# Kernel optimization log

Measured on AMD Instinct MI355X. Metric: run time of the kernel, lower is better.

The kernel has to match this reference:

```python
import jax, jax.numpy as jnp
import numpy as np

N_NODES = 100000


def gcn_conv(x, W, b, src, dst, n_nodes):
    # PyG GCNConv: x' = D^{-1/2} (A + I) D^{-1/2} (x W) + b, deg counts self-loops
    h = x @ W  # [N, out]
    deg = jax.ops.segment_sum(jnp.ones_like(dst, dtype=h.dtype), dst, num_segments=n_nodes) + 1.0
    dinv = jax.lax.rsqrt(deg)  # [N]
    norm = dinv[src] * dinv[dst]  # per-edge norm [E]
    msg = h[src] * norm[:, None]  # gather + scale, [E, out]
    agg = jax.ops.segment_sum(msg, dst, num_segments=n_nodes)
    agg = agg + h * (dinv * dinv)[:, None]  # self-loop contribution
    return agg + b


def setup_inputs() -> dict:
    key = jax.random.key(0)
    ks = jax.random.split(key, 9)
    N, E, D = N_NODES, 3200000, 165
    x = jax.random.normal(ks[0], (N, D), dtype=jnp.float32)
    edge_index = jax.random.randint(ks[1], (2, E), 0, N, dtype=jnp.int64)
    def glorot(k, fan_in, fan_out):
        lim = np.sqrt(6.0 / (fan_in + fan_out))
        return jax.random.uniform(k, (fan_in, fan_out), jnp.float32, -lim, lim)
    return {
        "x": x,
        "edge_index": edge_index,
        "W1": glorot(ks[2], D, 32), "b1": jnp.zeros((32,), jnp.float32),
        "W2": glorot(ks[3], 32, 16), "b2": jnp.zeros((16,), jnp.float32),
        "W3": glorot(ks[4], 16, 2),  "b3": jnp.zeros((2,), jnp.float32),
    }


def reference(x, edge_index, W1, b1, W2, b2, W3, b3):
    src, dst = edge_index[0], edge_index[1]
    n = x.shape[0]
    h = jax.nn.relu(gcn_conv(x, W1, b1, src, dst, n))
    # dropout p=0.3 is a no-op in eval mode (training=False)
    h = jax.nn.relu(gcn_conv(h, W2, b2, src, dst, n))
    h = gcn_conv(h, W3, b3, src, dst, n)
    return jax.nn.log_softmax(h, axis=1)
```

## Files before the change

### kernel.cpp

```cpp
#include <hip/hip_runtime.h>
#include <math.h>


constexpr int NT = 256;
constexpr int NPB = 256;
constexpr int LOG_NPB = 8;
constexpr int MAXBUK = 512;
constexpr int BSTRIDE = 10240;
constexpr int NREP = 8;
constexpr int SUB = BSTRIDE / NREP;
constexpr int EPB_B = 4096;
constexpr int R = 8;
constexpr int RSH = 14;

typedef __attribute__((ext_vector_type(8))) short bf16x8;
typedef __attribute__((ext_vector_type(4))) float f32x4;

__device__ inline unsigned short f2bf(float f) {
    unsigned u = *(unsigned*)&f;
    u += 0x7fffu + ((u >> 16) & 1u);
    return (unsigned short)(u >> 16);
}
__device__ inline unsigned packbf(float a, float b) {
    return (unsigned)f2bf(a) | ((unsigned)f2bf(b) << 16);
}
__device__ inline void acc8(float* a, uint4 v) {
    const unsigned* u = (const unsigned*)&v;
#pragma unroll
    for (int w = 0; w < 4; w++) {
        unsigned lo = u[w] << 16, hi = u[w] & 0xffff0000u;
        a[2 * w]     += *(float*)&lo;
        a[2 * w + 1] += *(float*)&hi;
    }
}

__global__ __launch_bounds__(NT) void place_kernel(const int* __restrict__ src,
                                                   const int* __restrict__ dst,
                                                   int* __restrict__ cursor8,
                                                   unsigned* __restrict__ ebuf,
                                                   int E, int nbuk) {
    __shared__ int lh[MAXBUK];
    __shared__ int lbase[MAXBUK];
    for (int i = threadIdx.x; i < nbuk; i += NT) lh[i] = 0;
    __syncthreads();
    constexpr int EPT = EPB_B / NT;
    unsigned pk[EPT];
    unsigned bl[EPT];
    int base = blockIdx.x * EPB_B;
    int rep = blockIdx.x & (NREP - 1);
#pragma unroll
    for (int i = 0; i < EPT; i++) {
        int e = base + i * NT + threadIdx.x;
        if (e < E) {
            int s = src[e], d = dst[e];
            int b = d >> LOG_NPB;
            int lp = atomicAdd(&lh[b], 1);
            pk[i] = ((unsigned)(d & (NPB - 1)) << 24) | (unsigned)s;
            bl[i] = ((unsigned)b << 16) | (unsigned)lp;
        } else {
            bl[i] = 0xFFFFFFFFu;
        }
    }
    __syncthreads();
    for (int i = threadIdx.x; i < nbuk; i += NT) {
        int v = lh[i];
        if (v) lbase[i] = atomicAdd(&cursor8[rep * MAXBUK + i], v);
    }
    __syncthreads();
#pragma unroll
    for (int i = 0; i < EPT; i++) {
        if (bl[i] != 0xFFFFFFFFu) {
            int b = (int)(bl[i] >> 16);
            int pos = lbase[b] + (int)(bl[i] & 0xFFFFu);
            if (pos < SUB)
                ebuf[(size_t)b * BSTRIDE + rep * SUB + pos] = pk[i];
        }
    }
}

__global__ __launch_bounds__(NT) void sort_kernel(
    const unsigned* __restrict__ ebuf, const int* __restrict__ cursor8,
    int* __restrict__ esrc, int* __restrict__ rowptr, int* __restrict__ rowcnt,
    float* __restrict__ dinv, int N) {
    __shared__ unsigned se[BSTRIDE];
    __shared__ int cnt[NPB * R];
    __shared__ int cur[NPB * R];
    __shared__ int psum[NT];
    int tid = threadIdx.x;
    int b = blockIdx.x;
    for (int i = tid; i < NPB * R; i += NT) cnt[i] = 0;
    __syncthreads();
    int scnt[NREP], sofs[NREP];
    int total = 0;
#pragma unroll
    for (int r = 0; r < NREP; r++) {
        int v = min(cursor8[r * MAXBUK + b], SUB);
        scnt[r] = v; sofs[r] = total; total += v;
    }
#pragma unroll
    for (int r = 0; r < NREP; r++) {
        int e0 = b * BSTRIDE + r * SUB;
        for (int i = tid; i < scnt[r]; i += NT) {
            unsigned p = ebuf[e0 + i];
            se[sofs[r] + i] = p;
            atomicAdd(&cnt[(p >> 24) * R + ((p & 0xFFFFFFu) >> RSH)], 1);
        }
    }
    __syncthreads();
    int loc[R];
    int s = 0;
#pragma unroll
    for (int i = 0; i < R; i++) { loc[i] = s; s += cnt[tid * R + i]; }
    psum[tid] = s;
    __syncthreads();
    for (int off = 1; off < NPB; off <<= 1) {
        int a = (tid >= off) ? psum[tid - off] : 0;
        __syncthreads();
        psum[tid] += a;
        __syncthreads();
    }
    int excl = psum[tid] - s;
#pragma unroll
    for (int i = 0; i < R; i++) cur[tid * R + i] = excl + loc[i];
    {
        int n = b * NPB + tid;
        if (n < N) {
            rowptr[n] = b * BSTRIDE + excl;
            rowcnt[n] = s;
            dinv[n] = rsqrtf((float)s + 1.0f);
        }
    }
    __syncthreads();
    for (int i = tid; i < total; i += NT) {
        unsigned p = se[i];
        unsigned sidx = p & 0xFFFFFFu;
        int bin = (int)(p >> 24) * R + (int)(sidx >> RSH);
        int pos = atomicAdd(&cur[bin], 1);
        esrc[b * BSTRIDE + pos] = (int)sidx;
    }
}

__global__ __launch_bounds__(NT) void gemm1_mfma(
    const float* __restrict__ in, const float* __restrict__ W,
    const float* __restrict__ dinv, uint4* __restrict__ hs, int Ntot) {
    constexpr int DIN = 165;
    constexpr int RP = 200;
    __shared__ unsigned short xs[64 * RP];
    __shared__ unsigned short ws[32 * RP];
    __shared__ float tile[4][16][36];
    int ntiles = (Ntot + 15) >> 4;
    int slab0 = (blockIdx.x * 4) << 4;
    int rows = min(64, Ntot - slab0);
    for (int i = threadIdx.x; i < (64 + 32) * (RP - DIN); i += NT) {
        int r = i / (RP - DIN);
        int k = DIN + (i - r * (RP - DIN));
        if (r < 64) xs[r * RP + k] = 0;
        else        ws[(r - 64) * RP + k] = 0;
    }
    {
        const float* xbase = in + (size_t)slab0 * DIN;
        int tot = rows * DIN;
        for (int i = threadIdx.x; i < tot; i += NT) {
            int r = i / DIN;
            xs[i + r * (RP - DIN)] = f2bf(xbase[i]);
        }
    }
    for (int i = threadIdx.x; i < DIN * 32; i += NT) {
        int k = i >> 5;
        int col = i & 31;
        ws[col * RP + k] = f2bf(W[i]);
    }
    __syncthreads();
    int lane = threadIdx.x & 63;
    int wv = threadIdx.x >> 6;
    int t = blockIdx.x * 4 + wv;
    if (t >= ntiles) return;
    int n0 = t << 4;
    int mrow = lane & 15;
    int quad = lane >> 4;
    int arow = n0 + mrow;
    if (arow >= Ntot) arow = Ntot - 1;
    int lrow = arow - slab0;
    f32x4 acc0 = {0.f, 0.f, 0.f, 0.f};
    f32x4 acc1 = {0.f, 0.f, 0.f, 0.f};
#pragma unroll
    for (int c = 0; c < 6; c++) {
        int kb = c * 32 + quad * 8;
        union { bf16x8 v; unsigned short u[8]; } A, B0, B1;
        __builtin_memcpy(&A.v,  &xs[lrow * RP + kb], 16);
        __builtin_memcpy(&B0.v, &ws[mrow * RP + kb], 16);
        __builtin_memcpy(&B1.v, &ws[(16 + mrow) * RP + kb], 16);
        acc0 = __builtin_amdgcn_mfma_f32_16x16x32_bf16(A.v, B0.v, acc0, 0, 0, 0);
        acc1 = __builtin_amdgcn_mfma_f32_16x16x32_bf16(A.v, B1.v, acc1, 0, 0, 0);
    }
#pragma unroll
    for (int r = 0; r < 4; r++) {
        tile[wv][quad * 4 + r][mrow] = acc0[r];
        tile[wv][quad * 4 + r][16 + mrow] = acc1[r];
    }
    int node = lane >> 2;
    int part = lane & 3;
    int n = n0 + node;
    if (n >= Ntot) return;
    float dv = dinv[n];
    float f[8];
#pragma unroll
    for (int i = 0; i < 8; i++) f[i] = tile[wv][node][part * 8 + i];
    unsigned u0 = packbf(dv * f[0], dv * f[1]);
    unsigned u1 = packbf(dv * f[2], dv * f[3]);
    unsigned u2 = packbf(dv * f[4], dv * f[5]);
    unsigned u3 = packbf(dv * f[6], dv * f[7]);
    hs[(size_t)n * 4 + part] = make_uint4(u0, u1, u2, u3);
}

__global__ __launch_bounds__(NT) void g1g2_kernel(
    const uint4* __restrict__ hsb, const int* __restrict__ esrc,
    const int* __restrict__ rowptr, const int* __restrict__ rowcnt,
    const float* __restrict__ dinv, const float* __restrict__ b1,
    const float* __restrict__ W2 , uint4* __restrict__ hs2b,
    int N) {
    __shared__ float sW[32 * 16];
    __shared__ float sb[32];
    for (int i = threadIdx.x; i < 32 * 16; i += NT) sW[i] = W2[i];
    if (threadIdx.x < 32) sb[threadIdx.x] = b1[threadIdx.x];
    __syncthreads();
    int gid = blockIdx.x * NT + threadIdx.x;
    int n = gid >> 2;
    int q = gid & 3;
    int c = q & 1;
    int h = q >> 1;
    if (n >= N) return;
    int start = rowptr[n];
    int cnt = rowcnt[n];
    int half0 = (cnt + 1) >> 1;
    int j    = start + (h ? half0 : 0);
    int jend = start + (h ? cnt : half0);
    float a[16];
    if (h == 0) {
        const uint4* hp = hsb + (size_t)n * 4 + c * 2;
        uint4 v0 = hp[0], v1 = hp[1];
        const unsigned* u0 = (const unsigned*)&v0;
        const unsigned* u1 = (const unsigned*)&v1;
#pragma unroll
        for (int w = 0; w < 4; w++) {
            unsigned lo = u0[w] << 16, hi = u0[w] & 0xffff0000u;
            a[2 * w] = *(float*)&lo; a[2 * w + 1] = *(float*)&hi;
            unsigned lo1 = u1[w] << 16, hi1 = u1[w] & 0xffff0000u;
            a[8 + 2 * w] = *(float*)&lo1; a[8 + 2 * w + 1] = *(float*)&hi1;
        }
    } else {
#pragma unroll
        for (int k = 0; k < 16; k++) a[k] = 0.f;
    }
    for (; j + 3 < jend; j += 4) {
        int s0 = esrc[j], s1 = esrc[j + 1], s2 = esrc[j + 2], s3 = esrc[j + 3];
        uint4 v00 = hsb[(size_t)s0 * 4 + c * 2], v01 = hsb[(size_t)s0 * 4 + c * 2 + 1];
        uint4 v10 = hsb[(size_t)s1 * 4 + c * 2], v11 = hsb[(size_t)s1 * 4 + c * 2 + 1];
        uint4 v20 = hsb[(size_t)s2 * 4 + c * 2], v21 = hsb[(size_t)s2 * 4 + c * 2 + 1];
        uint4 v30 = hsb[(size_t)s3 * 4 + c * 2], v31 = hsb[(size_t)s3 * 4 + c * 2 + 1];
        acc8(a, v00); acc8(a + 8, v01);
        acc8(a, v10); acc8(a + 8, v11);
        acc8(a, v20); acc8(a + 8, v21);
        acc8(a, v30); acc8(a + 8, v31);
    }
    for (; j < jend; j++) {
        int s = esrc[j];
        acc8(a, hsb[(size_t)s * 4 + c * 2]);
        acc8(a + 8, hsb[(size_t)s * 4 + c * 2 + 1]);
    }
#pragma unroll
    for (int k = 0; k < 16; k++) a[k] += __shfl_xor(a[k], 2);
    float dv = dinv[n];
    float z[16];
#pragma unroll
    for (int d = 0; d < 16; d++) z[d] = 0.f;
#pragma unroll
    for (int k = 0; k < 16; k++) {
        float f = fmaxf(fmaf(dv, a[k], sb[c * 16 + k]), 0.f);
#pragma unroll
        for (int d = 0; d < 16; d++)
            z[d] = fmaf(f, sW[(c * 16 + k) * 16 + d], z[d]);
    }
#pragma unroll
    for (int d = 0; d < 16; d++) z[d] += __shfl_xor(z[d], 1);
    if (h == 0) {
        unsigned u0 = packbf(dv * z[c * 8 + 0], dv * z[c * 8 + 1]);
        unsigned u1 = packbf(dv * z[c * 8 + 2], dv * z[c * 8 + 3]);
        unsigned u2 = packbf(dv * z[c * 8 + 4], dv * z[c * 8 + 5]);
        unsigned u3 = packbf(dv * z[c * 8 + 6], dv * z[c * 8 + 7]);
        hs2b[(size_t)n * 2 + c] = make_uint4(u0, u1, u2, u3);
    }
}

__global__ __launch_bounds__(NT) void g2g3_kernel(
    const uint4* __restrict__ hs2b, const int* __restrict__ esrc,
    const int* __restrict__ rowptr, const int* __restrict__ rowcnt,
    const float* __restrict__ dinv, const float* __restrict__ b2,
    const float* __restrict__ W3 , float* __restrict__ hs3,
    int N) {
    __shared__ float sW[32];
    __shared__ float sb[16];
    if (threadIdx.x < 32) sW[threadIdx.x] = W3[threadIdx.x];
    if (threadIdx.x < 16) sb[threadIdx.x] = b2[threadIdx.x];
    __syncthreads();
    int gid = blockIdx.x * NT + threadIdx.x;
    int n = gid >> 2;
    int q = gid & 3;
    int c = q & 1;
    int h = q >> 1;
    if (n >= N) return;
    int start = rowptr[n];
    int cnt = rowcnt[n];
    int half0 = (cnt + 1) >> 1;
    int j    = start + (h ? half0 : 0);
    int jend = start + (h ? cnt : half0);
    float a[8];
    if (h == 0) {
        uint4 v = hs2b[(size_t)n * 2 + c];
        const unsigned* u = (const unsigned*)&v;
#pragma unroll
        for (int w = 0; w < 4; w++) {
            unsigned lo = u[w] << 16, hi = u[w] & 0xffff0000u;
            a[2 * w] = *(float*)&lo; a[2 * w + 1] = *(float*)&hi;
        }
    } else {
#pragma unroll
        for (int k = 0; k < 8; k++) a[k] = 0.f;
    }
    for (; j + 3 < jend; j += 4) {
        uint4 v0 = hs2b[(size_t)esrc[j] * 2 + c];
        uint4 v1 = hs2b[(size_t)esrc[j + 1] * 2 + c];
        uint4 v2 = hs2b[(size_t)esrc[j + 2] * 2 + c];
        uint4 v3 = hs2b[(size_t)esrc[j + 3] * 2 + c];
        acc8(a, v0); acc8(a, v1); acc8(a, v2); acc8(a, v3);
    }
    for (; j < jend; j++) acc8(a, hs2b[(size_t)esrc[j] * 2 + c]);
#pragma unroll
    for (int k = 0; k < 8; k++) a[k] += __shfl_xor(a[k], 2);
    float dv = dinv[n];
    float z0 = 0.f, z1 = 0.f;
#pragma unroll
    for (int k = 0; k < 8; k++) {
        float f = fmaxf(fmaf(dv, a[k], sb[c * 8 + k]), 0.f);
        z0 = fmaf(f, sW[(c * 8 + k) * 2 + 0], z0);
        z1 = fmaf(f, sW[(c * 8 + k) * 2 + 1], z1);
    }
    z0 += __shfl_xor(z0, 1);
    z1 += __shfl_xor(z1, 1);
    if (q == 0) {
        hs3[(size_t)n * 2 + 0] = dv * z0;
        hs3[(size_t)n * 2 + 1] = dv * z1;
    }
}

__global__ __launch_bounds__(NT) void final_kernel(
    const float* __restrict__ hs3, const int* __restrict__ esrc,
    const int* __restrict__ rowptr, const int* __restrict__ rowcnt,
    const float* __restrict__ dinv, const float* __restrict__ b,
    float* __restrict__ out, int N) {
    int gid = blockIdx.x * NT + threadIdx.x;
    int n = gid >> 1;
    int h = gid & 1;
    if (n >= N) return;
    int start = rowptr[n];
    int cnt = rowcnt[n];
    int half0 = (cnt + 1) >> 1;
    int j    = start + (h ? half0 : 0);
    int jend = start + (h ? cnt : half0);
    const float2* h2 = (const float2*)hs3;
    float2 acc = h ? make_float2(0.f, 0.f) : h2[n];
    for (; j + 3 < jend; j += 4) {
        float2 v0 = h2[esrc[j]], v1 = h2[esrc[j + 1]];
        float2 v2 = h2[esrc[j + 2]], v3 = h2[esrc[j + 3]];
        acc.x += v0.x + v1.x + v2.x + v3.x;
        acc.y += v0.y + v1.y + v2.y + v3.y;
    }
    for (; j < jend; j++) {
        float2 v = h2[esrc[j]];
        acc.x += v.x; acc.y += v.y;
    }
    acc.x += __shfl_xor(acc.x, 1);
    acc.y += __shfl_xor(acc.y, 1);
    if (h == 0) {
        float dv = dinv[n];
        float z0 = fmaf(dv, acc.x, b[0]);
        float z1 = fmaf(dv, acc.y, b[1]);
        float m = fmaxf(z0, z1);
        float lse = m + logf(expf(z0 - m) + expf(z1 - m));
        out[(size_t)n * 2 + 0] = z0 - lse;
        out[(size_t)n * 2 + 1] = z1 - lse;
    }
}

extern "C" void kernel_launch(void* const* d_in, const int* in_sizes, int n_in,
                              void* d_out, int out_size, void* d_ws, size_t ws_size,
                              hipStream_t stream) {
    const float* x  = (const float*)d_in[0];
    const int*   ei = (const int*)d_in[1];
    const float* W1 = (const float*)d_in[2];
    const float* b1 = (const float*)d_in[3];
    const float* W2 = (const float*)d_in[4];
    const float* b2 = (const float*)d_in[5];
    const float* W3 = (const float*)d_in[6];
    const float* b3 = (const float*)d_in[7];
    float* out = (float*)d_out;

    const int N = in_sizes[0] / 165;
    const int E = in_sizes[1] / 2;
    const int* src = ei;
    const int* dst = ei + E;
    const int nbuk = (N + NPB - 1) >> LOG_NPB;
    const int G4 = ((size_t)N * 4 + NT - 1) / NT;
    const int G2 = ((size_t)N * 2 + NT - 1) / NT;

    char* p = (char*)d_ws;
    int* cursor8   = (int*)p;      p += (size_t)NREP * MAXBUK * 4;
    unsigned* ebuf = (unsigned*)p; p += (size_t)nbuk * BSTRIDE * 4;
    int* esrc      = (int*)p;      p += (size_t)nbuk * BSTRIDE * 4;
    int* rowptr    = (int*)p;      p += (size_t)N * 4;
    int* rowcnt    = (int*)p;      p += (size_t)N * 4;
    float* dinv    = (float*)p;    p += (size_t)N * 4;
    uint4* hs1b    = (uint4*)p;    p += (size_t)N * 4 * 16;
    uint4* hs2b    = (uint4*)p;    p += (size_t)N * 2 * 16;
    float* hs3     = (float*)p;    p += (size_t)N * 2 * 4;

    (void)hipMemsetAsync(cursor8, 0, (size_t)NREP * MAXBUK * sizeof(int), stream);
    place_kernel<<<(E + EPB_B - 1) / EPB_B, NT, 0, stream>>>(src, dst, cursor8, ebuf, E, nbuk);
    sort_kernel<<<nbuk, NT, 0, stream>>>(ebuf, cursor8, esrc, rowptr, rowcnt, dinv, N);

    gemm1_mfma<<<((N + 15) / 16 + 3) / 4, NT, 0, stream>>>(x, W1, dinv, hs1b, N);

    g1g2_kernel<<<G4, NT, 0, stream>>>(hs1b, esrc, rowptr, rowcnt, dinv, b1, W2, hs2b, N);

    g2g3_kernel<<<G4, NT, 0, stream>>>(hs2b, esrc, rowptr, rowcnt, dinv, b2, W3, hs3, N);

    final_kernel<<<G2, NT, 0, stream>>>(hs3, esrc, rowptr, rowcnt, dinv, b3, out, N);
}
```

Measured before the change: 278.6 us.

## Phase layer-1 gather by source-node range for cache locality

sort_kernel now also writes eight per-node sub-range offsets, one for each source-index bin (source >> 14). The layer-1 aggregation walks these bins in four phases, each followed by a block barrier, so threads in a block gather from the same slice of the feature table at the same time and cache hits should rise. The two half-threads of a node now take interleaved bins instead of the two halves of the edge list. Out-of-range threads are clamped to the last node rather than returning, so they can reach the barriers. This costs an extra 32 bytes per node of offset traffic, adds barrier stalls, and the clamped threads do redundant work and write the same values again.

```diff
diff --git a/kernel.cpp b/kernel.cpp
--- a/kernel.cpp
+++ b/kernel.cpp
@@ -81,7 +81,7 @@
 __global__ __launch_bounds__(NT) void sort_kernel(
     const unsigned* __restrict__ ebuf, const int* __restrict__ cursor8,
     int* __restrict__ esrc, int* __restrict__ rowptr, int* __restrict__ rowcnt,
-    float* __restrict__ dinv, int N) {
+    int* __restrict__ rowptr8, float* __restrict__ dinv, int N) {
     __shared__ unsigned se[BSTRIDE];
     __shared__ int cnt[NPB * R];
     __shared__ int cur[NPB * R];
@@ -128,6 +128,9 @@
             rowptr[n] = b * BSTRIDE + excl;
             rowcnt[n] = s;
             dinv[n] = rsqrtf((float)s + 1.0f);
+#pragma unroll
+            for (int i = 0; i < R; i++)
+                rowptr8[(size_t)n * 8 + i] = b * BSTRIDE + excl + loc[i];
         }
     }
     __syncthreads();
@@ -215,7 +218,7 @@
 
 __global__ __launch_bounds__(NT) void g1g2_kernel(
     const uint4* __restrict__ hsb, const int* __restrict__ esrc,
-    const int* __restrict__ rowptr, const int* __restrict__ rowcnt,
+    const int* __restrict__ rowptr8, const int* __restrict__ rowcnt,
     const float* __restrict__ dinv, const float* __restrict__ b1,
     const float* __restrict__ W2 , uint4* __restrict__ hs2b,
     int N) {
@@ -229,12 +232,15 @@
     int q = gid & 3;
     int c = q & 1;
     int h = q >> 1;
-    if (n >= N) return;
-    int start = rowptr[n];
-    int cnt = rowcnt[n];
-    int half0 = (cnt + 1) >> 1;
-    int j    = start + (h ? half0 : 0);
-    int jend = start + (h ? cnt : half0);
+    bool alive = (n < N);
+    if (!alive) n = N - 1;
+    int rp[9];
+    {
+        const int* rpp = rowptr8 + (size_t)n * 8;
+#pragma unroll
+        for (int i = 0; i < 8; i++) rp[i] = rpp[i];
+        rp[8] = rp[0] + rowcnt[n];
+    }
     float a[16];
     if (h == 0) {
         const uint4* hp = hsb + (size_t)n * 4 + c * 2;
@@ -252,21 +258,26 @@
 #pragma unroll
         for (int k = 0; k < 16; k++) a[k] = 0.f;
     }
-    for (; j + 3 < jend; j += 4) {
-        int s0 = esrc[j], s1 = esrc[j + 1], s2 = esrc[j + 2], s3 = esrc[j + 3];
-        uint4 v00 = hsb[(size_t)s0 * 4 + c * 2], v01 = hsb[(size_t)s0 * 4 + c * 2 + 1];
-        uint4 v10 = hsb[(size_t)s1 * 4 + c * 2], v11 = hsb[(size_t)s1 * 4 + c * 2 + 1];
-        uint4 v20 = hsb[(size_t)s2 * 4 + c * 2], v21 = hsb[(size_t)s2 * 4 + c * 2 + 1];
-        uint4 v30 = hsb[(size_t)s3 * 4 + c * 2], v31 = hsb[(size_t)s3 * 4 + c * 2 + 1];
-        acc8(a, v00); acc8(a + 8, v01);
-        acc8(a, v10); acc8(a + 8, v11);
-        acc8(a, v20); acc8(a + 8, v21);
-        acc8(a, v30); acc8(a + 8, v31);
-    }
-    for (; j < jend; j++) {
-        int s = esrc[j];
-        acc8(a, hsb[(size_t)s * 4 + c * 2]);
-        acc8(a + 8, hsb[(size_t)s * 4 + c * 2 + 1]);
+    for (int k = 0; k < 4; k++) {
+        int w = 2 * k + h;
+        int j = rp[w], jend = rp[w + 1];
+        for (; j + 3 < jend; j += 4) {
+            int s0 = esrc[j], s1 = esrc[j + 1], s2 = esrc[j + 2], s3 = esrc[j + 3];
+            uint4 v00 = hsb[(size_t)s0 * 4 + c * 2], v01 = hsb[(size_t)s0 * 4 + c * 2 + 1];
+            uint4 v10 = hsb[(size_t)s1 * 4 + c * 2], v11 = hsb[(size_t)s1 * 4 + c * 2 + 1];
+            uint4 v20 = hsb[(size_t)s2 * 4 + c * 2], v21 = hsb[(size_t)s2 * 4 + c * 2 + 1];
+            uint4 v30 = hsb[(size_t)s3 * 4 + c * 2], v31 = hsb[(size_t)s3 * 4 + c * 2 + 1];
+            acc8(a, v00); acc8(a + 8, v01);
+            acc8(a, v10); acc8(a + 8, v11);
+            acc8(a, v20); acc8(a + 8, v21);
+            acc8(a, v30); acc8(a + 8, v31);
+        }
+        for (; j < jend; j++) {
+            int s = esrc[j];
+            acc8(a, hsb[(size_t)s * 4 + c * 2]);
+            acc8(a + 8, hsb[(size_t)s * 4 + c * 2 + 1]);
+        }
+        __syncthreads();
     }
 #pragma unroll
     for (int k = 0; k < 16; k++) a[k] += __shfl_xor(a[k], 2);
@@ -419,6 +430,7 @@
     int* esrc      = (int*)p;      p += (size_t)nbuk * BSTRIDE * 4;
     int* rowptr    = (int*)p;      p += (size_t)N * 4;
     int* rowcnt    = (int*)p;      p += (size_t)N * 4;
+    int* rowptr8   = (int*)p;      p += (size_t)N * 8 * 4;
     float* dinv    = (float*)p;    p += (size_t)N * 4;
     uint4* hs1b    = (uint4*)p;    p += (size_t)N * 4 * 16;
     uint4* hs2b    = (uint4*)p;    p += (size_t)N * 2 * 16;
@@ -426,11 +438,11 @@
 
     (void)hipMemsetAsync(cursor8, 0, (size_t)NREP * MAXBUK * sizeof(int), stream);
     place_kernel<<<(E + EPB_B - 1) / EPB_B, NT, 0, stream>>>(src, dst, cursor8, ebuf, E, nbuk);
-    sort_kernel<<<nbuk, NT, 0, stream>>>(ebuf, cursor8, esrc, rowptr, rowcnt, dinv, N);
+    sort_kernel<<<nbuk, NT, 0, stream>>>(ebuf, cursor8, esrc, rowptr, rowcnt, rowptr8, dinv, N);
 
     gemm1_mfma<<<((N + 15) / 16 + 3) / 4, NT, 0, stream>>>(x, W1, dinv, hs1b, N);
 
-    g1g2_kernel<<<G4, NT, 0, stream>>>(hs1b, esrc, rowptr, rowcnt, dinv, b1, W2, hs2b, N);
+    g1g2_kernel<<<G4, NT, 0, stream>>>(hs1b, esrc, rowptr8, rowcnt, dinv, b1, W2, hs2b, N);
 
     g2g3_kernel<<<G4, NT, 0, stream>>>(hs2b, esrc, rowptr, rowcnt, dinv, b2, W3, hs3, N);
 
```

Result: slower. 286.0 us (+2.6%).
